# Performance work log

Hardware: AMD Instinct MI355X
Metric: run time of the kernel (lower is better)

Reference implementation:

```python
import jax, jax.numpy as jnp
import numpy as np

B, D, H, E, C, TOPK = 16384, 2048, 2048, 6, 1024, 3

def setup_inputs() -> dict:
    key = jax.random.key(0)
    ks = jax.random.split(key, 8)
    s_d = 1.0 / np.sqrt(D)
    s_h = 1.0 / np.sqrt(H)
    return {
        "x": jax.random.normal(ks[0], (B, D), dtype=jnp.float32),
        "gate_W": jax.random.uniform(ks[1], (E, D), jnp.float32, -s_d, s_d),
        "gate_b": jax.random.uniform(ks[2], (E,), jnp.float32, -s_d, s_d),
        "W1": jax.random.uniform(ks[3], (E, H, D), jnp.float32, -s_d, s_d),
        "b1": jax.random.uniform(ks[4], (E, H), jnp.float32, -s_d, s_d),
        "W2": jax.random.uniform(ks[5], (E, C, H), jnp.float32, -s_h, s_h),
        "b2": jax.random.uniform(ks[6], (E, C), jnp.float32, -s_h, s_h),
    }

def reference(x, gate_W, gate_b, W1, b1, W2, b2):
    # gating: top-k sparse softmax
    gate_logits = x @ gate_W.T + gate_b                      # [B, E]
    topk_vals, topk_idx = jax.lax.top_k(gate_logits, TOPK)   # [B, K]
    neg_inf = jnp.finfo(gate_logits.dtype).min
    sparse = jnp.full_like(gate_logits, neg_inf)
    rows = jnp.arange(gate_logits.shape[0])[:, None]
    sparse = sparse.at[rows, topk_idx].set(topk_vals)
    gw = jax.nn.softmax(sparse, axis=-1)                     # [B, E]
    # dense experts: Linear -> GELU (exact, erf) -> Linear (dropout is eval no-op)
    h = jnp.einsum('bd,ehd->beh', x, W1) + b1[None]          # [B, E, H]
    h = jax.nn.gelu(h, approximate=False)
    expert_outs = jnp.einsum('beh,ech->bec', h, W2) + b2[None]  # [B, E, C]
    out = jnp.einsum('be,bec->bc', gw, expert_outs)          # masked combine
    return (out, gw)
```

## Files before the change

### kernel.cpp

```cpp
#include <hip/hip_runtime.h>
#include <hip/hip_bf16.h>
#include <math.h>

#define B_ 16384
#define D_ 2048
#define H_ 2048
#define E_ 6
#define C_ 1024

typedef __attribute__((ext_vector_type(8))) short short8;
typedef __attribute__((ext_vector_type(4))) float f32x4;

__device__ __forceinline__ unsigned short f2bf(float f) {
    __hip_bfloat16 h = __float2bfloat16(f);
    return *reinterpret_cast<unsigned short*>(&h);
}

__device__ __forceinline__ void async_copy16(const unsigned short* g, unsigned short* l) {
    __builtin_amdgcn_global_load_lds(
        (const __attribute__((address_space(1))) unsigned int*)(g),
        (__attribute__((address_space(3))) unsigned int*)(l), 16, 0, 0);
}

__global__ void gate_kernel(const float* __restrict__ x, const float* __restrict__ gW,
                            const float* __restrict__ gb, float* __restrict__ gw_out,
                            int* __restrict__ counts, int* __restrict__ rowlist,
                            float* __restrict__ wtslist, unsigned short* __restrict__ xb) {
    int wave = threadIdx.x >> 6;
    int lane = threadIdx.x & 63;
    int row  = blockIdx.x * 4 + wave;
    const float* xr = x + (size_t)row * D_;
    unsigned short* xbr = xb + (size_t)row * D_;
    double acc[E_] = {0, 0, 0, 0, 0, 0};
    for (int i = 0; i < D_ / 64; ++i) {
        int d = i * 64 + lane;
        float xf = xr[d];
        xbr[d] = f2bf(xf);
        double xv = (double)xf;
#pragma unroll
        for (int e = 0; e < E_; ++e) acc[e] += xv * (double)gW[e * D_ + d];
    }
#pragma unroll
    for (int off = 32; off > 0; off >>= 1) {
#pragma unroll
        for (int e = 0; e < E_; ++e) acc[e] += __shfl_down(acc[e], off);
    }
    if (lane == 0) {
        double lg[E_];
#pragma unroll
        for (int e = 0; e < E_; ++e) lg[e] = acc[e] + (double)gb[e];
        bool used[E_] = {false, false, false, false, false, false};
        int idx[3]; double val[3];
        for (int k = 0; k < 3; ++k) {
            int best = -1; double bv = -1e300;
            for (int e = 0; e < E_; ++e)
                if (!used[e] && lg[e] > bv) { bv = lg[e]; best = e; }
            used[best] = true; idx[k] = best; val[k] = bv;
        }
        double m = val[0];
        double w[3]; double s = 0.0;
        for (int k = 0; k < 3; ++k) { w[k] = exp(val[k] - m); s += w[k]; }
        float gwv[E_] = {0.f, 0.f, 0.f, 0.f, 0.f, 0.f};
        for (int k = 0; k < 3; ++k) gwv[idx[k]] = (float)(w[k] / s);
#pragma unroll
        for (int e = 0; e < E_; ++e) gw_out[(size_t)row * E_ + e] = gwv[e];
        for (int k = 0; k < 3; ++k) {
            int e = idx[k];
            int pos = atomicAdd(&counts[e], 1);
            rowlist[(size_t)e * B_ + pos] = row * 3 + k;
            wtslist[(size_t)e * B_ + pos] = (float)(w[k] / s);
        }
    }
}

__global__ void cast_f32_bf16(const float* __restrict__ in, unsigned short* __restrict__ out, int n4) {
    int i = blockIdx.x * blockDim.x + threadIdx.x;
    if (i < n4) {
        float4 v = ((const float4*)in)[i];
        ushort4 u;
        u.x = f2bf(v.x); u.y = f2bf(v.y); u.z = f2bf(v.z); u.w = f2bf(v.w);
        ((ushort4*)out)[i] = u;
    }
}


#define GEMM_CORE(KDIM)                                                          \
    int lane = tid & 63;                                                         \
    int wv   = tid >> 6;                                                         \
    int wr   = wv >> 2;                                       \
    int wc   = wv & 3;                                      \
    int fm   = lane & 15;                                                        \
    int kg   = lane >> 4;                                                        \
    int laneoff = ((fm >> 1) << 6) + ((((fm & 1) << 2) + kg) ^ ((fm >> 1) & 7)) * 8; \
    int aBase = wr * 4096 + laneoff;                                             \
    int bBase = wc * 2048 + laneoff;                                             \
    f32x4 acc[8][4] = {};                                                        \
    const int NT = (KDIM) / 32;                                                  \
    _Pragma("unroll")                                                            \
    for (int pt = 0; pt < 3; ++pt) {                                             \
        unsigned short* Ab = As + pt * 8192;                                     \
        unsigned short* Bb = Bs + pt * 8192;                                     \
        int k0 = pt * 32;                                                        \
        async_copy16(aptr[0] + k0, Ab + (0 * 512 + tid) * 8);                    \
        async_copy16(aptr[1] + k0, Ab + (1 * 512 + tid) * 8);                    \
        async_copy16(bptr[0] + k0, Bb + (0 * 512 + tid) * 8);                    \
        async_copy16(bptr[1] + k0, Bb + (1 * 512 + tid) * 8);                    \
    }                                                                            \
    asm volatile("s_waitcnt vmcnt(8)" ::: "memory");                             \
    __builtin_amdgcn_s_barrier();                                                \
    __builtin_amdgcn_sched_barrier(0);                                           \
    for (int t = 0; t < NT; ++t) {                                               \
        unsigned short* Ab = As + (t & 3) * 8192;                                \
        unsigned short* Bb = Bs + (t & 3) * 8192;                                \
        if (t + 3 < NT) {                                                        \
            unsigned short* An = As + ((t + 3) & 3) * 8192;                      \
            unsigned short* Bn = Bs + ((t + 3) & 3) * 8192;                      \
            int k0 = (t + 3) * 32;                                               \
            async_copy16(aptr[0] + k0, An + (0 * 512 + tid) * 8);                \
            async_copy16(aptr[1] + k0, An + (1 * 512 + tid) * 8);                \
            async_copy16(bptr[0] + k0, Bn + (0 * 512 + tid) * 8);                \
            async_copy16(bptr[1] + k0, Bn + (1 * 512 + tid) * 8);                \
        }                                                                        \
        short8 bF[4];                                                            \
        _Pragma("unroll")                                                        \
        for (int n = 0; n < 4; ++n)                                              \
            bF[n] = *(const short8*)(Bb + bBase + n * 512);                      \
        _Pragma("unroll")                                                        \
        for (int m = 0; m < 8; ++m) {                                            \
            short8 aF = *(const short8*)(Ab + aBase + m * 512);                  \
            _Pragma("unroll")                                                    \
            for (int n = 0; n < 4; ++n)                                          \
                acc[m][n] = __builtin_amdgcn_mfma_f32_16x16x32_bf16(             \
                    aF, bF[n], acc[m][n], 0, 0, 0);                              \
        }                                                                        \
        if (t + 3 < NT)      asm volatile("s_waitcnt vmcnt(8)" ::: "memory");    \
        else if (t + 2 < NT) asm volatile("s_waitcnt vmcnt(4)" ::: "memory");    \
        else                 asm volatile("s_waitcnt vmcnt(0)" ::: "memory");    \
        __builtin_amdgcn_s_barrier();                                            \
        __builtin_amdgcn_sched_barrier(0);                                       \
    }

#define SLOT_DECODE(s, R, g)                                                     \
    int rr_##R = (s) >> 3;                                                       \
    int pp_##R = ((s) & 7) ^ (rr_##R & 7);                                       \
    int R = 2 * rr_##R + (pp_##R >> 2);                                          \
    int g = pp_##R & 3;

__global__ __launch_bounds__(512, 2) void gemm1_kernel(
    const unsigned short* __restrict__ xb, const unsigned short* __restrict__ W1b,
    const float* __restrict__ b1, const int* __restrict__ counts,
    const int* __restrict__ rowlist, unsigned short* __restrict__ hbuf) {
    int e = blockIdx.z;
    int cnt = counts[e];
    int flat = blockIdx.x;
    int p  = (flat & 7) + ((flat >> 6) << 3);
    int nb = (flat >> 3) & 7;
    int m0 = p * 256;
    if (m0 >= cnt) return;
    int n0 = nb * 256;

    __shared__ __align__(16) unsigned short As[4 * 8192];
    __shared__ __align__(16) unsigned short Bs[4 * 8192];
    int tid = threadIdx.x;
    const int* rlist = rowlist + (size_t)e * B_;

    const unsigned short* aptr[2];
    const unsigned short* bptr[2];
#pragma unroll
    for (int it = 0; it < 2; ++it) {
        int s = it * 512 + tid;
        SLOT_DECODE(s, Ra, ga)
        int idx = m0 + Ra; if (idx >= cnt) idx = cnt - 1;
        aptr[it] = xb + (size_t)(rlist[idx] / 3) * D_ + ga * 8;
        bptr[it] = W1b + (size_t)e * H_ * D_ + (size_t)(n0 + Ra) * D_ + ga * 8;
    }

    GEMM_CORE(D_)

    int rlim = cnt - m0;
#pragma unroll
    for (int m = 0; m < 8; ++m) {
#pragma unroll
        for (int i = 0; i < 4; ++i) {
            int r = wr * 128 + m * 16 + kg * 4 + i;
            if (r < rlim) {
                size_t base = (size_t)rlist[m0 + r] * H_ + n0;
#pragma unroll
                for (int n = 0; n < 4; ++n) {
                    int col = wc * 64 + n * 16 + fm;
                    float v = acc[m][n][i] + b1[e * H_ + n0 + col];
                    v = 0.5f * v * (1.0f + erff(v * 0.70710678118654752f));
                    hbuf[base + col] = f2bf(v);
                }
            }
        }
    }
}

__global__ __launch_bounds__(512, 2) void gemm2_kernel(
    const unsigned short* __restrict__ hbuf, const unsigned short* __restrict__ W2b,
    const float* __restrict__ b2, const int* __restrict__ counts,
    const int* __restrict__ rowlist, const float* __restrict__ wtslist,
    float* __restrict__ sbuf, float* __restrict__ out) {
    int e = blockIdx.z;
    int cnt = counts[e];
    int flat = blockIdx.x;
    int p  = (flat & 7) + ((flat >> 5) << 3);
    int nb = (flat >> 3) & 3;
    int m0 = p * 256;
    if (m0 >= cnt) return;
    int n0 = nb * 256;

    __shared__ __align__(16) unsigned short As[4 * 8192];
    __shared__ __align__(16) unsigned short Bs[4 * 8192];
    int tid = threadIdx.x;
    const int* rlist = rowlist + (size_t)e * B_;
    const float* wlist = wtslist + (size_t)e * B_;

    const unsigned short* aptr[2];
    const unsigned short* bptr[2];
#pragma unroll
    for (int it = 0; it < 2; ++it) {
        int s = it * 512 + tid;
        SLOT_DECODE(s, Ra, ga)
        int idx = m0 + Ra; if (idx >= cnt) idx = cnt - 1;
        aptr[it] = hbuf + (size_t)rlist[idx] * H_ + ga * 8;
        bptr[it] = W2b + (size_t)e * C_ * H_ + (size_t)(n0 + Ra) * H_ + ga * 8;
    }

    GEMM_CORE(H_)

    int rlim = cnt - m0;
#pragma unroll
    for (int m = 0; m < 8; ++m) {
#pragma unroll
        for (int i = 0; i < 4; ++i) {
            int r = wr * 128 + m * 16 + kg * 4 + i;
            if (r < rlim) {
                int slot = rlist[m0 + r];
                float w  = wlist[m0 + r];
                if (sbuf) {
                    float* srow = sbuf + (size_t)slot * C_ + n0;
#pragma unroll
                    for (int n = 0; n < 4; ++n) {
                        int col = wc * 64 + n * 16 + fm;
                        srow[col] = (acc[m][n][i] + b2[e * C_ + n0 + col]) * w;
                    }
                } else {
                    float* orow = out + (size_t)(slot / 3) * C_ + n0;
#pragma unroll
                    for (int n = 0; n < 4; ++n) {
                        int col = wc * 64 + n * 16 + fm;
                        atomicAdd(&orow[col], (acc[m][n][i] + b2[e * C_ + n0 + col]) * w);
                    }
                }
            }
        }
    }
}

__global__ void combine_kernel(const float* __restrict__ sbuf, float* __restrict__ out) {
    int i   = blockIdx.x * 256 + threadIdx.x;
    int row = i >> 8;
    int c4  = i & 255;
    const float4* s4 = (const float4*)sbuf;
    size_t b = (size_t)row * 3 * 256 + c4;
    float4 a = s4[b], d = s4[b + 256], g = s4[b + 512];
    float4 r;
    r.x = a.x + d.x + g.x; r.y = a.y + d.y + g.y;
    r.z = a.z + d.z + g.z; r.w = a.w + d.w + g.w;
    ((float4*)out)[i] = r;
}

extern "C" void kernel_launch(void* const* d_in, const int* in_sizes, int n_in,
                              void* d_out, int out_size, void* d_ws, size_t ws_size,
                              hipStream_t stream) {
    const float* x  = (const float*)d_in[0];
    const float* gW = (const float*)d_in[1];
    const float* gb = (const float*)d_in[2];
    const float* W1 = (const float*)d_in[3];
    const float* b1 = (const float*)d_in[4];
    const float* W2 = (const float*)d_in[5];
    const float* b2 = (const float*)d_in[6];
    float* out    = (float*)d_out;
    float* gw_out = out + (size_t)B_ * C_;

    char* ws = (char*)d_ws;
    size_t off = 0;
    auto alloc = [&](size_t bytes) -> char* {
        char* p = ws + off;
        off = (off + bytes + 255) & ~(size_t)255;
        return p;
    };
    int*            counts  = (int*)alloc(E_ * 4);
    int*            rowlist = (int*)alloc((size_t)E_ * B_ * 4);
    float*          wtslist = (float*)alloc((size_t)E_ * B_ * 4);
    unsigned short* W2b     = (unsigned short*)alloc((size_t)E_ * C_ * H_ * 2);
    unsigned short* hbuf    = (unsigned short*)alloc((size_t)3 * B_ * H_ * 2);
    size_t region_off = off;
    unsigned short* xb      = (unsigned short*)alloc((size_t)B_ * D_ * 2);
    unsigned short* W1b     = (unsigned short*)alloc((size_t)E_ * H_ * D_ * 2);
    float*          sbuf    = (float*)(ws + region_off);
    size_t sbuf_end = region_off + (size_t)3 * B_ * C_ * 4;
    bool use_sbuf = (ws_size == 0) || (sbuf_end <= ws_size);
    (void)in_sizes; (void)n_in; (void)out_size;

    hipMemsetAsync(counts, 0, E_ * 4, stream);
    if (!use_sbuf) hipMemsetAsync(out, 0, (size_t)B_ * C_ * 4, stream);

    gate_kernel<<<B_ / 4, 256, 0, stream>>>(x, gW, gb, gw_out, counts, rowlist, wtslist, xb);
    cast_f32_bf16<<<(E_ * H_ * D_ / 4) / 256, 256, 0, stream>>>(W1, W1b, E_ * H_ * D_ / 4);
    cast_f32_bf16<<<(E_ * C_ * H_ / 4) / 256, 256, 0, stream>>>(W2, W2b, E_ * C_ * H_ / 4);
    gemm1_kernel<<<dim3(8 * (B_ / 256), 1, E_), 512, 0, stream>>>(xb, W1b, b1, counts, rowlist, hbuf);
    gemm2_kernel<<<dim3(4 * (B_ / 256), 1, E_), 512, 0, stream>>>(hbuf, W2b, b2, counts, rowlist, wtslist,
                                                                  use_sbuf ? sbuf : (float*)nullptr, out);
    if (use_sbuf)
        combine_kernel<<<(B_ * C_ / 4) / 256, 256, 0, stream>>>(sbuf, out);
}
```

Before: 2.050 ms.

## Restructure GEMM mainloop into double-buffered K=64 tiles with phased MFMA interleaving

The shared GEMM core moves from a 4-stage ring of K=32 tiles to a 2-stage double buffer of K=64 tiles, with a new XOR-swizzled LDS layout split into row halves. Each iteration is split into four MFMA phases separated by barriers and s_setprio. LDS fragment reads and the next tile's global-to-LDS copies are issued between phases so memory traffic overlaps the matrix math. The aim is fewer barriers per unit of K and better MFMA/load overlap, at the cost of a shallower prefetch depth and more barriers inside each iteration.

New measurement: 1.873 ms. 8.7% less time.

```diff
diff --git a/kernel.cpp b/kernel.cpp
--- a/kernel.cpp
+++ b/kernel.cpp
@@ -7,6 +7,8 @@
 #define H_ 2048
 #define E_ 6
 #define C_ 1024
+
+#define HALF_ (128 * 64)
 
 typedef __attribute__((ext_vector_type(8))) short short8;
 typedef __attribute__((ext_vector_type(4))) float f32x4;
@@ -84,67 +86,132 @@
 }
 
 
+#define PHASE_IN()                                                               \
+    __builtin_amdgcn_sched_barrier(0);                                           \
+    __builtin_amdgcn_s_barrier();                                                \
+    asm volatile("s_waitcnt lgkmcnt(0)" ::: "memory");                           \
+    __builtin_amdgcn_sched_barrier(0);                                           \
+    __builtin_amdgcn_s_setprio(1);
+
+#define PHASE_OUT()                                                              \
+    __builtin_amdgcn_s_setprio(0);                                               \
+    __builtin_amdgcn_sched_barrier(0);                                           \
+    __builtin_amdgcn_s_barrier();
+
+#define STAGE_A(dstbuf, koff)                                                    \
+    _Pragma("unroll")                                                            \
+    for (int h_ = 0; h_ < 2; ++h_)                                               \
+        _Pragma("unroll")                                                        \
+        for (int j_ = 0; j_ < 2; ++j_)                                           \
+            async_copy16(asrc[h_][j_] + (koff),                                  \
+                         (dstbuf) + h_ * HALF_ + (j_ * 512 + tid) * 8);
+
+#define STAGE_B(dstbuf, koff)                                                    \
+    _Pragma("unroll")                                                            \
+    for (int h_ = 0; h_ < 2; ++h_)                                               \
+        _Pragma("unroll")                                                        \
+        for (int j_ = 0; j_ < 2; ++j_)                                           \
+            async_copy16(bsrc[h_][j_] + (koff),                                  \
+                         (dstbuf) + h_ * HALF_ + (j_ * 512 + tid) * 8);
+
+#define MFMA_BF16 __builtin_amdgcn_mfma_f32_16x16x32_bf16
+
 #define GEMM_CORE(KDIM)                                                          \
     int lane = tid & 63;                                                         \
-    int wv   = tid >> 6;                                                         \
-    int wr   = wv >> 2;                                       \
-    int wc   = wv & 3;                                      \
-    int fm   = lane & 15;                                                        \
-    int kg   = lane >> 4;                                                        \
-    int laneoff = ((fm >> 1) << 6) + ((((fm & 1) << 2) + kg) ^ ((fm >> 1) & 7)) * 8; \
-    int aBase = wr * 4096 + laneoff;                                             \
-    int bBase = wc * 2048 + laneoff;                                             \
+    int wv = tid >> 6;                                                           \
+    int wr = wv >> 2;                                        \
+    int wc = wv & 3;                                         \
+    int fm = lane & 15;                                                          \
+    int kg = lane >> 4;                                                          \
+    unsigned g0 = (unsigned)((kg ^ (fm & 7)) * 8);                               \
+    unsigned g1 = (unsigned)(((4 + kg) ^ (fm & 7)) * 8);                         \
+    unsigned aRB = (unsigned)(wr * HALF_ + fm * 64);                             \
+    unsigned bRB = (unsigned)((wc >> 1) * HALF_ + ((wc & 1) * 64 + fm) * 64);    \
     f32x4 acc[8][4] = {};                                                        \
-    const int NT = (KDIM) / 32;                                                  \
-    _Pragma("unroll")                                                            \
-    for (int pt = 0; pt < 3; ++pt) {                                             \
-        unsigned short* Ab = As + pt * 8192;                                     \
-        unsigned short* Bb = Bs + pt * 8192;                                     \
-        int k0 = pt * 32;                                                        \
-        async_copy16(aptr[0] + k0, Ab + (0 * 512 + tid) * 8);                    \
-        async_copy16(aptr[1] + k0, Ab + (1 * 512 + tid) * 8);                    \
-        async_copy16(bptr[0] + k0, Bb + (0 * 512 + tid) * 8);                    \
-        async_copy16(bptr[1] + k0, Bb + (1 * 512 + tid) * 8);                    \
-    }                                                                            \
+    const int NT = (KDIM) / 64;                                                  \
+    STAGE_A(As, 0) STAGE_B(Bs, 0)                                                \
+    STAGE_A(As + 2 * HALF_, 64) STAGE_B(Bs + 2 * HALF_, 64)                      \
     asm volatile("s_waitcnt vmcnt(8)" ::: "memory");                             \
     __builtin_amdgcn_s_barrier();                                                \
     __builtin_amdgcn_sched_barrier(0);                                           \
     for (int t = 0; t < NT; ++t) {                                               \
-        unsigned short* Ab = As + (t & 3) * 8192;                                \
-        unsigned short* Bb = Bs + (t & 3) * 8192;                                \
-        if (t + 3 < NT) {                                                        \
-            unsigned short* An = As + ((t + 3) & 3) * 8192;                      \
-            unsigned short* Bn = Bs + ((t + 3) & 3) * 8192;                      \
-            int k0 = (t + 3) * 32;                                               \
-            async_copy16(aptr[0] + k0, An + (0 * 512 + tid) * 8);                \
-            async_copy16(aptr[1] + k0, An + (1 * 512 + tid) * 8);                \
-            async_copy16(bptr[0] + k0, Bn + (0 * 512 + tid) * 8);                \
-            async_copy16(bptr[1] + k0, Bn + (1 * 512 + tid) * 8);                \
+        unsigned short* Ab = As + (t & 1) * (2 * HALF_);                         \
+        unsigned short* Bb = Bs + (t & 1) * (2 * HALF_);                         \
+        const bool st = (t + 2 < NT);                                            \
+        const int koff = (t + 2) * 64;                                           \
+        const unsigned short* Ar0 = Ab + aRB + g0;                               \
+        const unsigned short* Ar1 = Ab + aRB + g1;                               \
+        const unsigned short* Br0 = Bb + bRB + g0;                               \
+        const unsigned short* Br1 = Bb + bRB + g1;                               \
+        short8 aF[4][2], bQ[2][2], bR[2][2];                                     \
+                       \
+        _Pragma("unroll")                                                        \
+        for (int m = 0; m < 4; ++m) {                                            \
+            aF[m][0] = *(const short8*)(Ar0 + m * 1024);                         \
+            aF[m][1] = *(const short8*)(Ar1 + m * 1024);                         \
         }                                                                        \
-        short8 bF[4];                                                            \
-        _Pragma("unroll")                                                        \
-        for (int n = 0; n < 4; ++n)                                              \
-            bF[n] = *(const short8*)(Bb + bBase + n * 512);                      \
-        _Pragma("unroll")                                                        \
-        for (int m = 0; m < 8; ++m) {                                            \
-            short8 aF = *(const short8*)(Ab + aBase + m * 512);                  \
+        _Pragma("unroll")                                                        \
+        for (int n = 0; n < 2; ++n) {                                            \
+            bQ[n][0] = *(const short8*)(Br0 + n * 1024);                         \
+            bQ[n][1] = *(const short8*)(Br1 + n * 1024);                         \
+        }                                                                        \
+        PHASE_IN()                                                               \
+        _Pragma("unroll")                                                        \
+        for (int m = 0; m < 4; ++m)                                              \
             _Pragma("unroll")                                                    \
-            for (int n = 0; n < 4; ++n)                                          \
-                acc[m][n] = __builtin_amdgcn_mfma_f32_16x16x32_bf16(             \
-                    aF, bF[n], acc[m][n], 0, 0, 0);                              \
+            for (int n = 0; n < 2; ++n) {                                        \
+                acc[m][n] = MFMA_BF16(aF[m][0], bQ[n][0], acc[m][n], 0, 0, 0);   \
+                acc[m][n] = MFMA_BF16(aF[m][1], bQ[n][1], acc[m][n], 0, 0, 0);   \
+            }                                                                    \
+        PHASE_OUT()                                                              \
+                                 \
+        _Pragma("unroll")                                                        \
+        for (int n = 0; n < 2; ++n) {                                            \
+            bR[n][0] = *(const short8*)(Br0 + (2 + n) * 1024);                   \
+            bR[n][1] = *(const short8*)(Br1 + (2 + n) * 1024);                   \
         }                                                                        \
-        if (t + 3 < NT)      asm volatile("s_waitcnt vmcnt(8)" ::: "memory");    \
-        else if (t + 2 < NT) asm volatile("s_waitcnt vmcnt(4)" ::: "memory");    \
-        else                 asm volatile("s_waitcnt vmcnt(0)" ::: "memory");    \
+        PHASE_IN()                                                               \
+        _Pragma("unroll")                                                        \
+        for (int m = 0; m < 4; ++m)                                              \
+            _Pragma("unroll")                                                    \
+            for (int n = 0; n < 2; ++n) {                                        \
+                acc[m][2 + n] = MFMA_BF16(aF[m][0], bR[n][0], acc[m][2 + n], 0, 0, 0); \
+                acc[m][2 + n] = MFMA_BF16(aF[m][1], bR[n][1], acc[m][2 + n], 0, 0, 0); \
+            }                                                                    \
+        PHASE_OUT()                                                               \
+                   \
+        _Pragma("unroll")                                                        \
+        for (int m = 0; m < 4; ++m) {                                            \
+            aF[m][0] = *(const short8*)(Ar0 + (4 + m) * 1024);                   \
+            aF[m][1] = *(const short8*)(Ar1 + (4 + m) * 1024);                   \
+        }                                                                        \
+        if (st) { STAGE_B(Bb, koff) }                                            \
+        PHASE_IN()                                                               \
+        _Pragma("unroll")                                                        \
+        for (int m = 0; m < 4; ++m)                                              \
+            _Pragma("unroll")                                                    \
+            for (int n = 0; n < 2; ++n) {                                        \
+                acc[4 + m][n] = MFMA_BF16(aF[m][0], bQ[n][0], acc[4 + m][n], 0, 0, 0); \
+                acc[4 + m][n] = MFMA_BF16(aF[m][1], bQ[n][1], acc[4 + m][n], 0, 0, 0); \
+            }                                                                    \
+        PHASE_OUT()                                                              \
+                 \
+        if (st) { STAGE_A(Ab, koff) }                                            \
+        PHASE_IN()                                                               \
+        _Pragma("unroll")                                                        \
+        for (int m = 0; m < 4; ++m)                                              \
+            _Pragma("unroll")                                                    \
+            for (int n = 0; n < 2; ++n) {                                        \
+                acc[4 + m][2 + n] = MFMA_BF16(aF[m][0], bR[n][0], acc[4 + m][2 + n], 0, 0, 0); \
+                acc[4 + m][2 + n] = MFMA_BF16(aF[m][1], bR[n][1], acc[4 + m][2 + n], 0, 0, 0); \
+            }                                                                    \
+        __builtin_amdgcn_s_setprio(0);                                           \
+        __builtin_amdgcn_sched_barrier(0);                                       \
+        if (st) asm volatile("s_waitcnt vmcnt(8)" ::: "memory");                 \
+        else    asm volatile("s_waitcnt vmcnt(0)" ::: "memory");                 \
         __builtin_amdgcn_s_barrier();                                            \
         __builtin_amdgcn_sched_barrier(0);                                       \
     }
-
-#define SLOT_DECODE(s, R, g)                                                     \
-    int rr_##R = (s) >> 3;                                                       \
-    int pp_##R = ((s) & 7) ^ (rr_##R & 7);                                       \
-    int R = 2 * rr_##R + (pp_##R >> 2);                                          \
-    int g = pp_##R & 3;
 
 __global__ __launch_bounds__(512, 2) void gemm1_kernel(
     const unsigned short* __restrict__ xb, const unsigned short* __restrict__ W1b,
@@ -159,21 +226,24 @@
     if (m0 >= cnt) return;
     int n0 = nb * 256;
 
-    __shared__ __align__(16) unsigned short As[4 * 8192];
-    __shared__ __align__(16) unsigned short Bs[4 * 8192];
+    __shared__ __align__(16) unsigned short As[4 * HALF_];
+    __shared__ __align__(16) unsigned short Bs[4 * HALF_];
     int tid = threadIdx.x;
     const int* rlist = rowlist + (size_t)e * B_;
 
-    const unsigned short* aptr[2];
-    const unsigned short* bptr[2];
-#pragma unroll
-    for (int it = 0; it < 2; ++it) {
-        int s = it * 512 + tid;
-        SLOT_DECODE(s, Ra, ga)
-        int idx = m0 + Ra; if (idx >= cnt) idx = cnt - 1;
-        aptr[it] = xb + (size_t)(rlist[idx] / 3) * D_ + ga * 8;
-        bptr[it] = W1b + (size_t)e * H_ * D_ + (size_t)(n0 + Ra) * D_ + ga * 8;
-    }
+    int rb = tid >> 3;
+    int gth = ((tid & 7) ^ (rb & 7)) * 8;
+    const unsigned short* asrc[2][2];
+    const unsigned short* bsrc[2][2];
+#pragma unroll
+    for (int h = 0; h < 2; ++h)
+#pragma unroll
+        for (int j = 0; j < 2; ++j) {
+            int r = h * 128 + j * 64 + rb;
+            int idx = m0 + r; if (idx >= cnt) idx = cnt - 1;
+            asrc[h][j] = xb + (size_t)(rlist[idx] / 3) * D_ + gth;
+            bsrc[h][j] = W1b + (size_t)e * H_ * D_ + (size_t)(n0 + r) * D_ + gth;
+        }
 
     GEMM_CORE(D_)
 
@@ -211,22 +281,25 @@
     if (m0 >= cnt) return;
     int n0 = nb * 256;
 
-    __shared__ __align__(16) unsigned short As[4 * 8192];
-    __shared__ __align__(16) unsigned short Bs[4 * 8192];
+    __shared__ __align__(16) unsigned short As[4 * HALF_];
+    __shared__ __align__(16) unsigned short Bs[4 * HALF_];
     int tid = threadIdx.x;
     const int* rlist = rowlist + (size_t)e * B_;
     const float* wlist = wtslist + (size_t)e * B_;
 
-    const unsigned short* aptr[2];
-    const unsigned short* bptr[2];
-#pragma unroll
-    for (int it = 0; it < 2; ++it) {
-        int s = it * 512 + tid;
-        SLOT_DECODE(s, Ra, ga)
-        int idx = m0 + Ra; if (idx >= cnt) idx = cnt - 1;
-        aptr[it] = hbuf + (size_t)rlist[idx] * H_ + ga * 8;
-        bptr[it] = W2b + (size_t)e * C_ * H_ + (size_t)(n0 + Ra) * H_ + ga * 8;
-    }
+    int rb = tid >> 3;
+    int gth = ((tid & 7) ^ (rb & 7)) * 8;
+    const unsigned short* asrc[2][2];
+    const unsigned short* bsrc[2][2];
+#pragma unroll
+    for (int h = 0; h < 2; ++h)
+#pragma unroll
+        for (int j = 0; j < 2; ++j) {
+            int r = h * 128 + j * 64 + rb;
+            int idx = m0 + r; if (idx >= cnt) idx = cnt - 1;
+            asrc[h][j] = hbuf + (size_t)rlist[idx] * H_ + gth;
+            bsrc[h][j] = W2b + (size_t)e * C_ * H_ + (size_t)(n0 + r) * H_ + gth;
+        }
 
     GEMM_CORE(H_)
 
```
